# Optimization experiments

Hardware: AMD Instinct MI355X
Metric: run time of the kernel (lower is better)

The kernel has to match this reference:

```python
import jax, jax.numpy as jnp
import numpy as np

N_NODES = 100000
N_EDGES = 3200000


def spmm(row, col, val, h):
    # sparse [N,N] @ dense [N,D] via gather + segment_sum
    msg = val[:, None] * h[col]  # [E, D]
    return jax.ops.segment_sum(msg, row, num_segments=N_NODES)


def setup_inputs() -> dict:
    key = jax.random.key(0)
    k1, k2, k3, k4, k5, k6 = jax.random.split(key, 6)
    x = jax.random.normal(k1, (N_NODES, 512), dtype=jnp.float32)
    W1 = jax.random.normal(k2, (512, 64), dtype=jnp.float32) * 0.05
    W2 = jax.random.normal(k3, (64, 40), dtype=jnp.float32) * 0.1
    adj_val = jax.random.uniform(k4, (N_EDGES,), dtype=jnp.float32)
    adj_row = jax.random.randint(k5, (N_EDGES,), 0, N_NODES, dtype=jnp.int32)
    adj_col = jax.random.randint(k6, (N_EDGES,), 0, N_NODES, dtype=jnp.int32)
    return {"x": x, "W1": W1, "W2": W2, "adj_val": adj_val,
            "adj_row": adj_row, "adj_col": adj_col}


def reference(x, W1, W2, adj_val, adj_row, adj_col):
    # Layer 1: XW1, then A @ (XW1), relu
    h = x @ W1                              # [N, 64]
    h = spmm(adj_row, adj_col, adj_val, h)  # [N, 64]
    h = jax.nn.relu(h)
    # Layer 2: HW2, then A @ (HW2)
    h = h @ W2                              # [N, 40]
    out = spmm(adj_row, adj_col, adj_val, h)
    return out
```

## Files before the change

### kernel.cpp

```cpp
#include <hip/hip_runtime.h>

#define N_NODES 100000
#define N_EDGES 3200000
#define CH      12500
#define C_NB    256
#define NBUCK   782
#define G1_NB   1563
#define BPAD    1024

typedef unsigned int uint;
typedef unsigned short ushort;

typedef __attribute__((ext_vector_type(8))) short short8;
typedef __attribute__((ext_vector_type(4))) float floatx4;

static __device__ __forceinline__ ushort f2bf(float f) {
    uint u = __float_as_uint(f);
    u += 0x7fffu + ((u >> 16) & 1u);
    return (ushort)(u >> 16);
}
static __device__ __forceinline__ float bf2f(ushort h) {
    return __uint_as_float(((uint)h) << 16);
}

__global__ __launch_bounds__(256) void prep_kernel(const float* __restrict__ W1,
                                                   ushort* __restrict__ W1f,
                                                   int* __restrict__ cc) {
    if (blockIdx.x < 128) {
        int t = blockIdx.x * 256 + threadIdx.x;
        int j = t & 7;
        int lane = (t >> 3) & 63;
        int tile = t >> 9;
        int kt = tile >> 2, nt = tile & 3;
        int k = kt * 32 + ((lane >> 4) << 3) + j;
        int n = nt * 16 + (lane & 15);
        W1f[t] = f2bf(W1[k * 64 + n]);
    } else {
        int i = (blockIdx.x - 128) * 256 + threadIdx.x;
        if (i < NBUCK) cc[i] = 0;
    }
}

__global__ __launch_bounds__(256) void fused_g1_c1_kernel(const float* __restrict__ X,
                                                          const ushort* __restrict__ W1f,
                                                          ushort* __restrict__ H1,
                                                          const int* __restrict__ row,
                                                          int* __restrict__ cc,
                                                          int* __restrict__ blockbase) {
    __shared__ int hist[NBUCK];
    if (blockIdx.x < C_NB) {
        const int blk = blockIdx.x;
        for (int i = threadIdx.x; i < NBUCK; i += 256) hist[i] = 0;
        __syncthreads();
        const int4* rp = reinterpret_cast<const int4*>(row + (long)blk * CH);
        for (int i = threadIdx.x; i < CH / 4; i += 256) {
            int4 r = rp[i];
            atomicAdd(&hist[r.x >> 7], 1);
            atomicAdd(&hist[r.y >> 7], 1);
            atomicAdd(&hist[r.z >> 7], 1);
            atomicAdd(&hist[r.w >> 7], 1);
        }
        __syncthreads();
        for (int i = threadIdx.x; i < NBUCK; i += 256) {
            int c = hist[i];
            int base = 0;
            if (c) base = atomicAdd(&cc[i], c);
            blockbase[blk * NBUCK + i] = base;
        }
    } else {
        const int bid = blockIdx.x - C_NB;
        const int tid = threadIdx.x;
        const int wave = tid >> 6;
        const int lane = tid & 63;
        const int arow = bid * 64 + wave * 16 + (lane & 15);
        const bool valid = arow < N_NODES;
        const float* xr = X + (long)arow * 512 + ((lane >> 4) << 3);
        const short8* bb = reinterpret_cast<const short8*>(W1f) + lane;

        floatx4 acc0 = {0.f, 0.f, 0.f, 0.f};
        floatx4 acc1 = {0.f, 0.f, 0.f, 0.f};
        floatx4 acc2 = {0.f, 0.f, 0.f, 0.f};
        floatx4 acc3 = {0.f, 0.f, 0.f, 0.f};

        for (int kt = 0; kt < 16; ++kt) {
            float4 ax0, ax1;
            if (valid) {
                ax0 = *reinterpret_cast<const float4*>(xr + kt * 32);
                ax1 = *reinterpret_cast<const float4*>(xr + kt * 32 + 4);
            } else {
                ax0 = make_float4(0.f, 0.f, 0.f, 0.f);
                ax1 = ax0;
            }
            uint4 ap;
            ap.x = (__float_as_uint(ax0.x) >> 16) | (__float_as_uint(ax0.y) & 0xffff0000u);
            ap.y = (__float_as_uint(ax0.z) >> 16) | (__float_as_uint(ax0.w) & 0xffff0000u);
            ap.z = (__float_as_uint(ax1.x) >> 16) | (__float_as_uint(ax1.y) & 0xffff0000u);
            ap.w = (__float_as_uint(ax1.z) >> 16) | (__float_as_uint(ax1.w) & 0xffff0000u);
            short8 a = *reinterpret_cast<short8*>(&ap);

            const short8* bk = bb + kt * 4 * 64;
            acc0 = __builtin_amdgcn_mfma_f32_16x16x32_bf16(a, bk[0 * 64], acc0, 0, 0, 0);
            acc1 = __builtin_amdgcn_mfma_f32_16x16x32_bf16(a, bk[1 * 64], acc1, 0, 0, 0);
            acc2 = __builtin_amdgcn_mfma_f32_16x16x32_bf16(a, bk[2 * 64], acc2, 0, 0, 0);
            acc3 = __builtin_amdgcn_mfma_f32_16x16x32_bf16(a, bk[3 * 64], acc3, 0, 0, 0);
        }

        const int mrow = bid * 64 + wave * 16 + (lane >> 4) * 4;
        const int ncol = lane & 15;
        #pragma unroll
        for (int r = 0; r < 4; ++r) {
            int orow = mrow + r;
            if (orow < N_NODES) {
                ushort* o = H1 + (long)orow * 64 + ncol;
                o[0]  = f2bf(acc0[r]);
                o[16] = f2bf(acc1[r]);
                o[32] = f2bf(acc2[r]);
                o[48] = f2bf(acc3[r]);
            }
        }
    }
}

__global__ __launch_bounds__(1024) void c2_scan_kernel(const int* __restrict__ cc,
                                                       int* __restrict__ cptr) {
    __shared__ int sm[1024];
    const int tid = threadIdx.x;
    int v = (tid < NBUCK) ? cc[tid] : 0;
    sm[tid] = v;
    __syncthreads();
    #pragma unroll
    for (int off = 1; off < 1024; off <<= 1) {
        int t = (tid >= off) ? sm[tid - off] : 0;
        __syncthreads();
        sm[tid] += t;
        __syncthreads();
    }
    if (tid < NBUCK) cptr[tid] = sm[tid] - v;
    if (tid == NBUCK - 1) cptr[NBUCK] = sm[tid];
}

__global__ __launch_bounds__(256) void c3_kernel(const int* __restrict__ row,
                                                 const int* __restrict__ col,
                                                 const float* __restrict__ val,
                                                 const int* __restrict__ cptr,
                                                 const int* __restrict__ blockbase,
                                                 int2* __restrict__ staging) {
    __shared__ int cnt[NBUCK];
    const int blk = blockIdx.x;
    for (int i = threadIdx.x; i < NBUCK; i += 256) cnt[i] = 0;
    __syncthreads();
    const long e0 = (long)blk * CH;
    const int4* rp = reinterpret_cast<const int4*>(row + e0);
    const int4* cp = reinterpret_cast<const int4*>(col + e0);
    const int4* vp = reinterpret_cast<const int4*>(reinterpret_cast<const int*>(val) + e0);
    const int* bb = blockbase + blk * NBUCK;
    for (int i = threadIdx.x; i < CH / 4; i += 256) {
        int4 r = rp[i];
        int4 c = cp[i];
        int4 v = vp[i];
        #pragma unroll
        for (int q = 0; q < 4; ++q) {
            int rr = (q == 0) ? r.x : (q == 1) ? r.y : (q == 2) ? r.z : r.w;
            int ccol = (q == 0) ? c.x : (q == 1) ? c.y : (q == 2) ? c.z : c.w;
            int vv = (q == 0) ? v.x : (q == 1) ? v.y : (q == 2) ? v.z : v.w;
            int b = rr >> 7;
            int lr = atomicAdd(&cnt[b], 1);
            int slot = cptr[b] + bb[b] + lr;
            staging[slot] = make_int2((ccol << 7) | (rr & 127), vv);
        }
    }
}

__global__ __launch_bounds__(256) void c4_kernel(const int* __restrict__ cptr,
                                                 const int2* __restrict__ staging,
                                                 int2* __restrict__ edges,
                                                 int* __restrict__ rowptr,
                                                 int* __restrict__ rowcnt) {
    __shared__ int cnt[128];
    __shared__ int sc[128];
    __shared__ int pexcl[129];
    __shared__ int cur[128];
    const int b = blockIdx.x;
    const int tid = threadIdx.x;
    const int lo = cptr[b], hi = cptr[b + 1];
    const int base = lo + BPAD * b;

    if (tid < 128) cnt[tid] = 0;
    __syncthreads();
    for (int i = lo + tid; i < hi; i += 256) atomicAdd(&cnt[staging[i].x & 127], 1);
    __syncthreads();
    int pv = 0;
    if (tid < 128) { pv = (cnt[tid] + 7) & ~7; sc[tid] = pv; }
    __syncthreads();
    #pragma unroll
    for (int off = 1; off < 128; off <<= 1) {
        int t = 0;
        if (tid < 128 && tid >= off) t = sc[tid - off];
        __syncthreads();
        if (tid < 128) sc[tid] += t;
        __syncthreads();
    }
    if (tid < 128) { pexcl[tid] = sc[tid] - pv; cur[tid] = sc[tid] - pv; }
    __syncthreads();
    if (tid < 128) {
        int gr = b * 128 + tid;
        if (gr < N_NODES) {
            rowptr[gr] = base + pexcl[tid];
            rowcnt[gr] = pv;
        }
        int s = base + pexcl[tid] + cnt[tid];
        int e = s + (pv - cnt[tid]);
        for (int i = s; i < e; ++i) edges[i] = make_int2(0, 0);
    }
    __syncthreads();
    for (int i = lo + tid; i < hi; i += 256) {
        int2 ev = staging[i];
        int pos = atomicAdd(&cur[ev.x & 127], 1);
        edges[base + pos] = make_int2(ev.x >> 7, ev.y);
    }
}

__global__ __launch_bounds__(256) void spmm1_w2_kernel(const int* __restrict__ rowptr,
                                                       const int* __restrict__ rowcnt,
                                                       const int2* __restrict__ edges,
                                                       const ushort* __restrict__ H1,
                                                       const float* __restrict__ W2,
                                                       ushort* __restrict__ H3) {
    __shared__ float Ws[64 * 40];
    __shared__ float hrow[4][64];
    for (int i = threadIdx.x; i < 64 * 40; i += 256) Ws[i] = W2[i];
    __syncthreads();

    const int r = blockIdx.x * 4 + (threadIdx.x >> 6);
    const int wave = threadIdx.x >> 6;
    const int lane = threadIdx.x & 63;
    if (r >= N_NODES) return;

    const int us = __builtin_amdgcn_readfirstlane(rowptr[r]);
    const int cnt8 = __builtin_amdgcn_readfirstlane(rowcnt[r]);
    const int2* __restrict__ ew = edges + us;

    float acc = 0.f;
    for (int j = 0; j < cnt8; j += 8) {
        int2 e0 = ew[j + 0], e1 = ew[j + 1], e2 = ew[j + 2], e3 = ew[j + 3];
        int2 e4 = ew[j + 4], e5 = ew[j + 5], e6 = ew[j + 6], e7 = ew[j + 7];
        ushort h0 = H1[e0.x * 64 + lane];
        ushort h1 = H1[e1.x * 64 + lane];
        ushort h2 = H1[e2.x * 64 + lane];
        ushort h3 = H1[e3.x * 64 + lane];
        ushort h4 = H1[e4.x * 64 + lane];
        ushort h5 = H1[e5.x * 64 + lane];
        ushort h6 = H1[e6.x * 64 + lane];
        ushort h7 = H1[e7.x * 64 + lane];
        acc = fmaf(__int_as_float(e0.y), bf2f(h0), acc);
        acc = fmaf(__int_as_float(e1.y), bf2f(h1), acc);
        acc = fmaf(__int_as_float(e2.y), bf2f(h2), acc);
        acc = fmaf(__int_as_float(e3.y), bf2f(h3), acc);
        acc = fmaf(__int_as_float(e4.y), bf2f(h4), acc);
        acc = fmaf(__int_as_float(e5.y), bf2f(h5), acc);
        acc = fmaf(__int_as_float(e6.y), bf2f(h6), acc);
        acc = fmaf(__int_as_float(e7.y), bf2f(h7), acc);
    }

    hrow[wave][lane] = fmaxf(acc, 0.f);
    float o = 0.f;
    if (lane < 40) {
        #pragma unroll
        for (int k = 0; k < 64; ++k) o += hrow[wave][k] * Ws[k * 40 + lane];
        H3[(long)r * 40 + lane] = f2bf(o);
    }
}

__global__ __launch_bounds__(256) void spmm2_kernel(const int* __restrict__ rowptr,
                                                    const int* __restrict__ rowcnt,
                                                    const int2* __restrict__ edges,
                                                    const ushort* __restrict__ H,
                                                    float* __restrict__ O) {
    const int r = blockIdx.x * 4 + (threadIdx.x >> 6);
    if (r >= N_NODES) return;
    const int lane = threadIdx.x & 63;

    const int us = __builtin_amdgcn_readfirstlane(rowptr[r]);
    const int cnt8 = __builtin_amdgcn_readfirstlane(rowcnt[r]);
    const int2* __restrict__ ew = edges + us;

    float acc = 0.f;
    for (int j = 0; j < cnt8; j += 8) {
        int2 e0 = ew[j + 0], e1 = ew[j + 1], e2 = ew[j + 2], e3 = ew[j + 3];
        int2 e4 = ew[j + 4], e5 = ew[j + 5], e6 = ew[j + 6], e7 = ew[j + 7];
        ushort h0 = H[e0.x * 40 + lane];
        ushort h1 = H[e1.x * 40 + lane];
        ushort h2 = H[e2.x * 40 + lane];
        ushort h3 = H[e3.x * 40 + lane];
        ushort h4 = H[e4.x * 40 + lane];
        ushort h5 = H[e5.x * 40 + lane];
        ushort h6 = H[e6.x * 40 + lane];
        ushort h7 = H[e7.x * 40 + lane];
        acc = fmaf(__int_as_float(e0.y), bf2f(h0), acc);
        acc = fmaf(__int_as_float(e1.y), bf2f(h1), acc);
        acc = fmaf(__int_as_float(e2.y), bf2f(h2), acc);
        acc = fmaf(__int_as_float(e3.y), bf2f(h3), acc);
        acc = fmaf(__int_as_float(e4.y), bf2f(h4), acc);
        acc = fmaf(__int_as_float(e5.y), bf2f(h5), acc);
        acc = fmaf(__int_as_float(e6.y), bf2f(h6), acc);
        acc = fmaf(__int_as_float(e7.y), bf2f(h7), acc);
    }
    if (lane < 40) O[(long)r * 40 + lane] = acc;
}

extern "C" void kernel_launch(void* const* d_in, const int* in_sizes, int n_in,
                              void* d_out, int out_size, void* d_ws, size_t ws_size,
                              hipStream_t stream) {
    const float* x       = (const float*)d_in[0];
    const float* W1      = (const float*)d_in[1];
    const float* W2      = (const float*)d_in[2];
    const float* adj_val = (const float*)d_in[3];
    const int*   adj_row = (const int*)d_in[4];
    const int*   adj_col = (const int*)d_in[5];
    float* out = (float*)d_out;

    char* ws = (char*)d_ws;
    const size_t OFF_H1     = 0;
    const size_t OFF_STG    = 12800000;
    const size_t OFF_H3     = 12800000;
    const size_t OFF_EDGES  = 38400000;
    const size_t OFF_ROWPTR = 70406272;
    const size_t OFF_ROWCNT = 70806272;
    const size_t OFF_CC     = 71206272;
    const size_t OFF_CPTR   = 71209408;
    const size_t OFF_BB     = 71212544;
    const size_t OFF_W1F    = 72013312;

    ushort* h1     = (ushort*)(ws + OFF_H1);
    int2*   stg    = (int2*)(ws + OFF_STG);
    ushort* h3     = (ushort*)(ws + OFF_H3);
    int2*   edges  = (int2*)(ws + OFF_EDGES);
    int*    rowptr = (int*)(ws + OFF_ROWPTR);
    int*    rowcnt = (int*)(ws + OFF_ROWCNT);
    int*    cc     = (int*)(ws + OFF_CC);
    int*    cptr   = (int*)(ws + OFF_CPTR);
    int*    bb     = (int*)(ws + OFF_BB);
    ushort* w1f    = (ushort*)(ws + OFF_W1F);

    prep_kernel<<<128 + 4, 256, 0, stream>>>(W1, w1f, cc);

    fused_g1_c1_kernel<<<C_NB + G1_NB, 256, 0, stream>>>(x, w1f, h1, adj_row, cc, bb);

    c2_scan_kernel<<<1, 1024, 0, stream>>>(cc, cptr);

    c3_kernel<<<C_NB, 256, 0, stream>>>(adj_row, adj_col, adj_val, cptr, bb, stg);

    c4_kernel<<<NBUCK, 256, 0, stream>>>(cptr, stg, edges, rowptr, rowcnt);

    spmm1_w2_kernel<<<(N_NODES + 3) / 4, 256, 0, stream>>>(rowptr, rowcnt, edges, h1, W2, h3);

    spmm2_kernel<<<(N_NODES + 3) / 4, 256, 0, stream>>>(rowptr, rowcnt, edges, h3, out);
}
```

Before: 308.0 us.

## Split GEMM1 across scatter and bucket-sort kernels to overlap with CSR build

Moves the X@W1 MFMA GEMM out of the histogram kernel and splits its blocks into two halves. One half is co-scheduled with the edge scatter (c3) and the other with the per-bucket sort (c4). The goal is to hide the latency-bound, atomic-heavy CSR construction phases behind bandwidth-heavy GEMM work, rather than overlapping GEMM only with the short histogram pass. The cost is that the histogram kernel now runs alone, and the GEMM blocks compete for resources with the scatter and sort blocks.

```diff
diff --git a/kernel.cpp b/kernel.cpp
--- a/kernel.cpp
+++ b/kernel.cpp
@@ -6,6 +6,7 @@
 #define C_NB    256
 #define NBUCK   782
 #define G1_NB   1563
+#define G1_HALF 782
 #define BPAD    1024
 
 typedef unsigned int uint;
@@ -21,6 +22,60 @@
 }
 static __device__ __forceinline__ float bf2f(ushort h) {
     return __uint_as_float(((uint)h) << 16);
+}
+
+static __device__ __forceinline__ void gemm1_block(int bid, int tid,
+                                                   const float* __restrict__ X,
+                                                   const ushort* __restrict__ W1f,
+                                                   ushort* __restrict__ H1) {
+    const int wave = tid >> 6;
+    const int lane = tid & 63;
+    const int arow = bid * 64 + wave * 16 + (lane & 15);
+    const bool valid = arow < N_NODES;
+    const float* xr = X + (long)arow * 512 + ((lane >> 4) << 3);
+    const short8* bb = reinterpret_cast<const short8*>(W1f) + lane;
+
+    floatx4 acc0 = {0.f, 0.f, 0.f, 0.f};
+    floatx4 acc1 = {0.f, 0.f, 0.f, 0.f};
+    floatx4 acc2 = {0.f, 0.f, 0.f, 0.f};
+    floatx4 acc3 = {0.f, 0.f, 0.f, 0.f};
+
+    for (int kt = 0; kt < 16; ++kt) {
+        float4 ax0, ax1;
+        if (valid) {
+            ax0 = *reinterpret_cast<const float4*>(xr + kt * 32);
+            ax1 = *reinterpret_cast<const float4*>(xr + kt * 32 + 4);
+        } else {
+            ax0 = make_float4(0.f, 0.f, 0.f, 0.f);
+            ax1 = ax0;
+        }
+        uint4 ap;
+        ap.x = (__float_as_uint(ax0.x) >> 16) | (__float_as_uint(ax0.y) & 0xffff0000u);
+        ap.y = (__float_as_uint(ax0.z) >> 16) | (__float_as_uint(ax0.w) & 0xffff0000u);
+        ap.z = (__float_as_uint(ax1.x) >> 16) | (__float_as_uint(ax1.y) & 0xffff0000u);
+        ap.w = (__float_as_uint(ax1.z) >> 16) | (__float_as_uint(ax1.w) & 0xffff0000u);
+        short8 a = *reinterpret_cast<short8*>(&ap);
+
+        const short8* bk = bb + kt * 4 * 64;
+        acc0 = __builtin_amdgcn_mfma_f32_16x16x32_bf16(a, bk[0 * 64], acc0, 0, 0, 0);
+        acc1 = __builtin_amdgcn_mfma_f32_16x16x32_bf16(a, bk[1 * 64], acc1, 0, 0, 0);
+        acc2 = __builtin_amdgcn_mfma_f32_16x16x32_bf16(a, bk[2 * 64], acc2, 0, 0, 0);
+        acc3 = __builtin_amdgcn_mfma_f32_16x16x32_bf16(a, bk[3 * 64], acc3, 0, 0, 0);
+    }
+
+    const int mrow = bid * 64 + wave * 16 + (lane >> 4) * 4;
+    const int ncol = lane & 15;
+    #pragma unroll
+    for (int r = 0; r < 4; ++r) {
+        int orow = mrow + r;
+        if (orow < N_NODES) {
+            ushort* o = H1 + (long)orow * 64 + ncol;
+            o[0]  = f2bf(acc0[r]);
+            o[16] = f2bf(acc1[r]);
+            o[32] = f2bf(acc2[r]);
+            o[48] = f2bf(acc3[r]);
+        }
+    }
 }
 
 __global__ __launch_bounds__(256) void prep_kernel(const float* __restrict__ W1,
@@ -41,83 +96,27 @@
     }
 }
 
-__global__ __launch_bounds__(256) void fused_g1_c1_kernel(const float* __restrict__ X,
-                                                          const ushort* __restrict__ W1f,
-                                                          ushort* __restrict__ H1,
-                                                          const int* __restrict__ row,
-                                                          int* __restrict__ cc,
-                                                          int* __restrict__ blockbase) {
+__global__ __launch_bounds__(256) void c1_kernel(const int* __restrict__ row,
+                                                 int* __restrict__ cc,
+                                                 int* __restrict__ blockbase) {
     __shared__ int hist[NBUCK];
-    if (blockIdx.x < C_NB) {
-        const int blk = blockIdx.x;
-        for (int i = threadIdx.x; i < NBUCK; i += 256) hist[i] = 0;
-        __syncthreads();
-        const int4* rp = reinterpret_cast<const int4*>(row + (long)blk * CH);
-        for (int i = threadIdx.x; i < CH / 4; i += 256) {
-            int4 r = rp[i];
-            atomicAdd(&hist[r.x >> 7], 1);
-            atomicAdd(&hist[r.y >> 7], 1);
-            atomicAdd(&hist[r.z >> 7], 1);
-            atomicAdd(&hist[r.w >> 7], 1);
-        }
-        __syncthreads();
-        for (int i = threadIdx.x; i < NBUCK; i += 256) {
-            int c = hist[i];
-            int base = 0;
-            if (c) base = atomicAdd(&cc[i], c);
-            blockbase[blk * NBUCK + i] = base;
-        }
-    } else {
-        const int bid = blockIdx.x - C_NB;
-        const int tid = threadIdx.x;
-        const int wave = tid >> 6;
-        const int lane = tid & 63;
-        const int arow = bid * 64 + wave * 16 + (lane & 15);
-        const bool valid = arow < N_NODES;
-        const float* xr = X + (long)arow * 512 + ((lane >> 4) << 3);
-        const short8* bb = reinterpret_cast<const short8*>(W1f) + lane;
-
-        floatx4 acc0 = {0.f, 0.f, 0.f, 0.f};
-        floatx4 acc1 = {0.f, 0.f, 0.f, 0.f};
-        floatx4 acc2 = {0.f, 0.f, 0.f, 0.f};
-        floatx4 acc3 = {0.f, 0.f, 0.f, 0.f};
-
-        for (int kt = 0; kt < 16; ++kt) {
-            float4 ax0, ax1;
-            if (valid) {
-                ax0 = *reinterpret_cast<const float4*>(xr + kt * 32);
-                ax1 = *reinterpret_cast<const float4*>(xr + kt * 32 + 4);
-            } else {
-                ax0 = make_float4(0.f, 0.f, 0.f, 0.f);
-                ax1 = ax0;
-            }
-            uint4 ap;
-            ap.x = (__float_as_uint(ax0.x) >> 16) | (__float_as_uint(ax0.y) & 0xffff0000u);
-            ap.y = (__float_as_uint(ax0.z) >> 16) | (__float_as_uint(ax0.w) & 0xffff0000u);
-            ap.z = (__float_as_uint(ax1.x) >> 16) | (__float_as_uint(ax1.y) & 0xffff0000u);
-            ap.w = (__float_as_uint(ax1.z) >> 16) | (__float_as_uint(ax1.w) & 0xffff0000u);
-            short8 a = *reinterpret_cast<short8*>(&ap);
-
-            const short8* bk = bb + kt * 4 * 64;
-            acc0 = __builtin_amdgcn_mfma_f32_16x16x32_bf16(a, bk[0 * 64], acc0, 0, 0, 0);
-            acc1 = __builtin_amdgcn_mfma_f32_16x16x32_bf16(a, bk[1 * 64], acc1, 0, 0, 0);
-            acc2 = __builtin_amdgcn_mfma_f32_16x16x32_bf16(a, bk[2 * 64], acc2, 0, 0, 0);
-            acc3 = __builtin_amdgcn_mfma_f32_16x16x32_bf16(a, bk[3 * 64], acc3, 0, 0, 0);
-        }
-
-        const int mrow = bid * 64 + wave * 16 + (lane >> 4) * 4;
-        const int ncol = lane & 15;
-        #pragma unroll
-        for (int r = 0; r < 4; ++r) {
-            int orow = mrow + r;
-            if (orow < N_NODES) {
-                ushort* o = H1 + (long)orow * 64 + ncol;
-                o[0]  = f2bf(acc0[r]);
-                o[16] = f2bf(acc1[r]);
-                o[32] = f2bf(acc2[r]);
-                o[48] = f2bf(acc3[r]);
-            }
-        }
+    const int blk = blockIdx.x;
+    for (int i = threadIdx.x; i < NBUCK; i += 256) hist[i] = 0;
+    __syncthreads();
+    const int4* rp = reinterpret_cast<const int4*>(row + (long)blk * CH);
+    for (int i = threadIdx.x; i < CH / 4; i += 256) {
+        int4 r = rp[i];
+        atomicAdd(&hist[r.x >> 7], 1);
+        atomicAdd(&hist[r.y >> 7], 1);
+        atomicAdd(&hist[r.z >> 7], 1);
+        atomicAdd(&hist[r.w >> 7], 1);
+    }
+    __syncthreads();
+    for (int i = threadIdx.x; i < NBUCK; i += 256) {
+        int c = hist[i];
+        int base = 0;
+        if (c) base = atomicAdd(&cc[i], c);
+        blockbase[blk * NBUCK + i] = base;
     }
 }
 
@@ -139,84 +138,98 @@
     if (tid == NBUCK - 1) cptr[NBUCK] = sm[tid];
 }
 
-__global__ __launch_bounds__(256) void c3_kernel(const int* __restrict__ row,
-                                                 const int* __restrict__ col,
-                                                 const float* __restrict__ val,
-                                                 const int* __restrict__ cptr,
-                                                 const int* __restrict__ blockbase,
-                                                 int2* __restrict__ staging) {
+__global__ __launch_bounds__(256) void fusedA_kernel(const int* __restrict__ row,
+                                                     const int* __restrict__ col,
+                                                     const float* __restrict__ val,
+                                                     const int* __restrict__ cptr,
+                                                     const int* __restrict__ blockbase,
+                                                     int2* __restrict__ staging,
+                                                     const float* __restrict__ X,
+                                                     const ushort* __restrict__ W1f,
+                                                     ushort* __restrict__ H1) {
     __shared__ int cnt[NBUCK];
-    const int blk = blockIdx.x;
-    for (int i = threadIdx.x; i < NBUCK; i += 256) cnt[i] = 0;
-    __syncthreads();
-    const long e0 = (long)blk * CH;
-    const int4* rp = reinterpret_cast<const int4*>(row + e0);
-    const int4* cp = reinterpret_cast<const int4*>(col + e0);
-    const int4* vp = reinterpret_cast<const int4*>(reinterpret_cast<const int*>(val) + e0);
-    const int* bb = blockbase + blk * NBUCK;
-    for (int i = threadIdx.x; i < CH / 4; i += 256) {
-        int4 r = rp[i];
-        int4 c = cp[i];
-        int4 v = vp[i];
-        #pragma unroll
-        for (int q = 0; q < 4; ++q) {
-            int rr = (q == 0) ? r.x : (q == 1) ? r.y : (q == 2) ? r.z : r.w;
-            int ccol = (q == 0) ? c.x : (q == 1) ? c.y : (q == 2) ? c.z : c.w;
-            int vv = (q == 0) ? v.x : (q == 1) ? v.y : (q == 2) ? v.z : v.w;
-            int b = rr >> 7;
-            int lr = atomicAdd(&cnt[b], 1);
-            int slot = cptr[b] + bb[b] + lr;
-            staging[slot] = make_int2((ccol << 7) | (rr & 127), vv);
-        }
-    }
-}
-
-__global__ __launch_bounds__(256) void c4_kernel(const int* __restrict__ cptr,
-                                                 const int2* __restrict__ staging,
-                                                 int2* __restrict__ edges,
-                                                 int* __restrict__ rowptr,
-                                                 int* __restrict__ rowcnt) {
+    if (blockIdx.x < C_NB) {
+        const int blk = blockIdx.x;
+        for (int i = threadIdx.x; i < NBUCK; i += 256) cnt[i] = 0;
+        __syncthreads();
+        const long e0 = (long)blk * CH;
+        const int4* rp = reinterpret_cast<const int4*>(row + e0);
+        const int4* cp = reinterpret_cast<const int4*>(col + e0);
+        const int4* vp = reinterpret_cast<const int4*>(reinterpret_cast<const int*>(val) + e0);
+        const int* bb = blockbase + blk * NBUCK;
+        for (int i = threadIdx.x; i < CH / 4; i += 256) {
+            int4 r = rp[i];
+            int4 c = cp[i];
+            int4 v = vp[i];
+            #pragma unroll
+            for (int q = 0; q < 4; ++q) {
+                int rr = (q == 0) ? r.x : (q == 1) ? r.y : (q == 2) ? r.z : r.w;
+                int ccol = (q == 0) ? c.x : (q == 1) ? c.y : (q == 2) ? c.z : c.w;
+                int vv = (q == 0) ? v.x : (q == 1) ? v.y : (q == 2) ? v.z : v.w;
+                int b = rr >> 7;
+                int lr = atomicAdd(&cnt[b], 1);
+                int slot = cptr[b] + bb[b] + lr;
+                staging[slot] = make_int2((ccol << 7) | (rr & 127), vv);
+            }
+        }
+    } else {
+        gemm1_block(blockIdx.x - C_NB, threadIdx.x, X, W1f, H1);
+    }
+}
+
+__global__ __launch_bounds__(256) void fusedB_kernel(const int* __restrict__ cptr,
+                                                     const int2* __restrict__ staging,
+                                                     int2* __restrict__ edges,
+                                                     int* __restrict__ rowptr,
+                                                     int* __restrict__ rowcnt,
+                                                     const float* __restrict__ X,
+                                                     const ushort* __restrict__ W1f,
+                                                     ushort* __restrict__ H1) {
     __shared__ int cnt[128];
     __shared__ int sc[128];
     __shared__ int pexcl[129];
     __shared__ int cur[128];
-    const int b = blockIdx.x;
-    const int tid = threadIdx.x;
-    const int lo = cptr[b], hi = cptr[b + 1];
-    const int base = lo + BPAD * b;
-
-    if (tid < 128) cnt[tid] = 0;
-    __syncthreads();
-    for (int i = lo + tid; i < hi; i += 256) atomicAdd(&cnt[staging[i].x & 127], 1);
-    __syncthreads();
-    int pv = 0;
-    if (tid < 128) { pv = (cnt[tid] + 7) & ~7; sc[tid] = pv; }
-    __syncthreads();
-    #pragma unroll
-    for (int off = 1; off < 128; off <<= 1) {
-        int t = 0;
-        if (tid < 128 && tid >= off) t = sc[tid - off];
-        __syncthreads();
-        if (tid < 128) sc[tid] += t;
-        __syncthreads();
-    }
-    if (tid < 128) { pexcl[tid] = sc[tid] - pv; cur[tid] = sc[tid] - pv; }
-    __syncthreads();
-    if (tid < 128) {
-        int gr = b * 128 + tid;
-        if (gr < N_NODES) {
-            rowptr[gr] = base + pexcl[tid];
-            rowcnt[gr] = pv;
-        }
-        int s = base + pexcl[tid] + cnt[tid];
-        int e = s + (pv - cnt[tid]);
-        for (int i = s; i < e; ++i) edges[i] = make_int2(0, 0);
-    }
-    __syncthreads();
-    for (int i = lo + tid; i < hi; i += 256) {
-        int2 ev = staging[i];
-        int pos = atomicAdd(&cur[ev.x & 127], 1);
-        edges[base + pos] = make_int2(ev.x >> 7, ev.y);
+    if (blockIdx.x < NBUCK) {
+        const int b = blockIdx.x;
+        const int tid = threadIdx.x;
+        const int lo = cptr[b], hi = cptr[b + 1];
+        const int base = lo + BPAD * b;
+
+        if (tid < 128) cnt[tid] = 0;
+        __syncthreads();
+        for (int i = lo + tid; i < hi; i += 256) atomicAdd(&cnt[staging[i].x & 127], 1);
+        __syncthreads();
+        int pv = 0;
+        if (tid < 128) { pv = (cnt[tid] + 7) & ~7; sc[tid] = pv; }
+        __syncthreads();
+        #pragma unroll
+        for (int off = 1; off < 128; off <<= 1) {
+            int t = 0;
+            if (tid < 128 && tid >= off) t = sc[tid - off];
+            __syncthreads();
+            if (tid < 128) sc[tid] += t;
+            __syncthreads();
+        }
+        if (tid < 128) { pexcl[tid] = sc[tid] - pv; cur[tid] = sc[tid] - pv; }
+        __syncthreads();
+        if (tid < 128) {
+            int gr = b * 128 + tid;
+            if (gr < N_NODES) {
+                rowptr[gr] = base + pexcl[tid];
+                rowcnt[gr] = pv;
+            }
+            int s = base + pexcl[tid] + cnt[tid];
+            int e = s + (pv - cnt[tid]);
+            for (int i = s; i < e; ++i) edges[i] = make_int2(0, 0);
+        }
+        __syncthreads();
+        for (int i = lo + tid; i < hi; i += 256) {
+            int2 ev = staging[i];
+            int pos = atomicAdd(&cur[ev.x & 127], 1);
+            edges[base + pos] = make_int2(ev.x >> 7, ev.y);
+        }
+    } else {
+        gemm1_block(G1_HALF + (blockIdx.x - NBUCK), threadIdx.x, X, W1f, H1);
     }
 }
 
@@ -344,13 +357,15 @@
 
     prep_kernel<<<128 + 4, 256, 0, stream>>>(W1, w1f, cc);
 
-    fused_g1_c1_kernel<<<C_NB + G1_NB, 256, 0, stream>>>(x, w1f, h1, adj_row, cc, bb);
+    c1_kernel<<<C_NB, 256, 0, stream>>>(adj_row, cc, bb);
 
     c2_scan_kernel<<<1, 1024, 0, stream>>>(cc, cptr);
 
-    c3_kernel<<<C_NB, 256, 0, stream>>>(adj_row, adj_col, adj_val, cptr, bb, stg);
-
-    c4_kernel<<<NBUCK, 256, 0, stream>>>(cptr, stg, edges, rowptr, rowcnt);
+    fusedA_kernel<<<C_NB + G1_HALF, 256, 0, stream>>>(adj_row, adj_col, adj_val,
+                                                      cptr, bb, stg, x, w1f, h1);
+
+    fusedB_kernel<<<NBUCK + (G1_NB - G1_HALF), 256, 0, stream>>>(cptr, stg, edges,
+                                                                 rowptr, rowcnt, x, w1f, h1);
 
     spmm1_w2_kernel<<<(N_NODES + 3) / 4, 256, 0, stream>>>(rowptr, rowcnt, edges, h1, W2, h3);
 
```

Measured after the change: 354.4 us. 15.1% more time.
